# Optimization experiments

Hardware: AMD Instinct MI355X
Metric: run time of the kernel (lower is better)

## Reference

```python
import jax, jax.numpy as jnp
import numpy as np

D_PRIME = 512
D = 2048
CLASSES = 4


def setup_inputs() -> dict:
    key = jax.random.key(0)
    k1, k2, k3, k4 = jax.random.split(key, 4)
    N = 32768
    V_prime = jax.random.normal(k1, (N, D), dtype=jnp.float32)
    U_t = jax.random.normal(k2, (D_PRIME, D), dtype=jnp.float32)
    W_mta = jax.random.normal(k3, (1, D_PRIME), dtype=jnp.float32)
    W = jax.random.normal(k4, (CLASSES, D), dtype=jnp.float32)
    return {"V_prime": V_prime, "U_t": U_t, "W_mta": W_mta, "W": W}


def reference(V_prime, U_t, W_mta, W):
    # [D_prime, N] = tanh(U_t @ V'^T)
    tanh_scores = jnp.tanh(U_t @ V_prime.T)
    # attention over instances: [1, N]
    a = jax.nn.softmax(W_mta @ tanh_scores, axis=1)
    # weighted sum pooling: [D]
    t = jnp.sum(a.T * V_prime, axis=0)
    # final linear: [1, classes]
    l = (W @ t).reshape(1, CLASSES)
    return l
```

## Files before the change

kernel.cpp:

```cpp
#include <hip/hip_runtime.h>

#define N_INST 32768
#define DIM    2048
#define DP     512
#define NCLS   4

typedef _Float16 half8_t  __attribute__((ext_vector_type(8)));
typedef float    float4_t __attribute__((ext_vector_type(4)));

#define OFF_UHI   0ull
#define OFF_S     (OFF_UHI  + (size_t)DP*DIM*2)
#define OFF_STAT  (OFF_S    + (size_t)N_INST*4)

__device__ __forceinline__ float tanh_fast(float x) {
  float e = __expf(2.0f * x);
  return 1.0f - 2.0f / (e + 1.0f);
}

typedef const unsigned int __attribute__((address_space(1)))* gas_t;
typedef unsigned int       __attribute__((address_space(3)))* las_t;
__device__ __forceinline__ void gl16(const void* g, void* l) {
  __builtin_amdgcn_global_load_lds((gas_t)g, (las_t)l, 16, 0, 0);
}

__global__ __launch_bounds__(256) void k_cvt(const float4* __restrict__ in,
                                             half8_t* __restrict__ out,
                                             float4* __restrict__ s4z) {
  int i = blockIdx.x * 256 + threadIdx.x;
  float4 a = in[2 * i], b = in[2 * i + 1];
  half8_t h;
  h[0] = (_Float16)a.x; h[1] = (_Float16)a.y;
  h[2] = (_Float16)a.z; h[3] = (_Float16)a.w;
  h[4] = (_Float16)b.x; h[5] = (_Float16)b.y;
  h[6] = (_Float16)b.z; h[7] = (_Float16)b.w;
  out[i] = h;
  if (i < N_INST / 4) s4z[i] = make_float4(0.f, 0.f, 0.f, 0.f);
}

__global__ __launch_bounds__(512, 2) void k_score_gemm(
    const _Float16* __restrict__ Uhi, const float* __restrict__ V,
    const float* __restrict__ Wmta, float* __restrict__ s) {
  __shared__ _Float16 lA[2][256 * 64];
  __shared__ _Float16 lB[2][256 * 64];

  const int tid  = threadIdx.x;
  const int lane = tid & 63;
  const int wv   = tid >> 6;
  const int waveM = wv >> 2;
  const int waveN = wv & 3;
  const int quad = lane >> 4;
  const int col  = lane & 15;

  const int b   = blockIdx.x;
  const int grp = b >> 4;
  const int win = b & 15;
  const int mb  = win >> 3;
  const int nb  = grp * 8 + (win & 7);

  const int aRow0  = mb * 256;
  const int bRow0  = nb * 256;
  const int kStart = (nb & 31) << 6;

  const int rsub = lane >> 3;
  const int sswz = (lane & 7) ^ rsub;
  const _Float16* gA[4];
  int dA[4];
#pragma unroll
  for (int i2 = 0; i2 < 4; ++i2) {
    const int c = wv * 4 + i2;
    gA[i2] = Uhi + (size_t)(aRow0 + c * 8 + rsub) * DIM + sswz * 8;
    dA[i2] = c * 512;
  }

  const int rw = tid >> 1;
  const int hw = tid & 1;
  const float* gB = V + (size_t)(bRow0 + rw) * DIM + hw * 32;
  int wOffB[4];
#pragma unroll
  for (int p = 0; p < 4; ++p)
    wOffB[p] = rw * 128 + ((((hw << 2) | p) ^ (rw & 7)) << 4);

  const int fsw = (quad ^ (col & 7)) << 4;
  int offA[8], offB[4];
#pragma unroll
  for (int mi = 0; mi < 8; ++mi)
    offA[mi] = (waveM * 128 + mi * 16 + col) * 128 + fsw;
#pragma unroll
  for (int ni = 0; ni < 4; ++ni)
    offB[ni] = (waveN * 64 + ni * 16 + col) * 128 + fsw;

  float4_t acc[8][4];
  const float4_t z4 = {0.f, 0.f, 0.f, 0.f};
#pragma unroll
  for (int i = 0; i < 8; i++)
#pragma unroll
    for (int j = 0; j < 4; j++) acc[i][j] = z4;

  float4 rb[8];

#define KOF(t) ((kStart + (t) * 64) & (DIM - 1))

#define LOADB(kk) do {                                                     \
    const float4* p4 = (const float4*)(gB + (kk));                         \
    _Pragma("unroll")                                                      \
    for (int j = 0; j < 8; ++j) rb[j] = p4[j];                             \
  } while (0)

#define WRITEB(CUR) do {                                                   \
    char* base = (char*)&lB[CUR][0];                                       \
    _Pragma("unroll")                                                      \
    for (int p = 0; p < 4; ++p) {                                          \
      const auto c0 = __builtin_amdgcn_cvt_pkrtz(rb[2*p].x,   rb[2*p].y);  \
      const auto c1 = __builtin_amdgcn_cvt_pkrtz(rb[2*p].z,   rb[2*p].w);  \
      const auto c2 = __builtin_amdgcn_cvt_pkrtz(rb[2*p+1].x, rb[2*p+1].y);\
      const auto c3 = __builtin_amdgcn_cvt_pkrtz(rb[2*p+1].z, rb[2*p+1].w);\
      half8_t h;                                                           \
      h[0] = (_Float16)c0[0]; h[1] = (_Float16)c0[1];                      \
      h[2] = (_Float16)c1[0]; h[3] = (_Float16)c1[1];                      \
      h[4] = (_Float16)c2[0]; h[5] = (_Float16)c2[1];                      \
      h[6] = (_Float16)c3[0]; h[7] = (_Float16)c3[1];                      \
      *(half8_t*)(base + wOffB[p]) = h;                                    \
    }                                                                      \
  } while (0)

#define STAGEA(CUR, kk) do {                                               \
    gl16(gA[0] + (kk), &lA[CUR][dA[0]]);                                   \
    gl16(gA[1] + (kk), &lA[CUR][dA[1]]);                                   \
    gl16(gA[2] + (kk), &lA[CUR][dA[2]]);                                   \
    gl16(gA[3] + (kk), &lA[CUR][dA[3]]);                                   \
  } while (0)

#define COMPUTE(CUR) do {                                                  \
    const char* pA = (const char*)&lA[CUR][0];                             \
    const char* pB = (const char*)&lB[CUR][0];                             \
    _Pragma("unroll")                                                      \
    for (int kh = 0; kh < 2; ++kh) {                                       \
      half8_t af[8], bf[4];                                                \
      _Pragma("unroll")                                                    \
      for (int mi = 0; mi < 8; ++mi)                                       \
        af[mi] = *(const half8_t*)(pA + (offA[mi] ^ (kh << 6)));           \
      _Pragma("unroll")                                                    \
      for (int ni = 0; ni < 4; ++ni)                                       \
        bf[ni] = *(const half8_t*)(pB + (offB[ni] ^ (kh << 6)));           \
      _Pragma("unroll")                                                    \
      for (int mi = 0; mi < 8; ++mi)                                       \
        _Pragma("unroll")                                                  \
        for (int ni = 0; ni < 4; ++ni)                                     \
          acc[mi][ni] = __builtin_amdgcn_mfma_f32_16x16x32_f16(            \
              af[mi], bf[ni], acc[mi][ni], 0, 0, 0);                       \
    }                                                                      \
  } while (0)

  LOADB(KOF(0));
  STAGEA(0, KOF(0));
  WRITEB(0);
  LOADB(KOF(1));
  __syncthreads();

  for (int t = 0; t < 32; t += 2) {
    if (t < 31)  { STAGEA(1, KOF(t + 1)); WRITEB(1); }
    if (t < 30)  LOADB(KOF(t + 2));
    COMPUTE(0);
    __syncthreads();
    if (t + 1 < 31) { STAGEA(0, KOF(t + 2)); WRITEB(0); }
    if (t + 1 < 30) LOADB(KOF(t + 3));
    COMPUTE(1);
    __syncthreads();
  }
#undef KOF
#undef LOADB
#undef WRITEB
#undef STAGEA
#undef COMPUTE

#pragma unroll
  for (int ni = 0; ni < 4; ni++) {
    float v = 0.0f;
#pragma unroll
    for (int mi = 0; mi < 8; mi++) {
      const int jb = aRow0 + waveM * 128 + mi * 16 + quad * 4;
      union { float4_t v4; float f[4]; } u;
      u.v4 = acc[mi][ni];
#pragma unroll
      for (int r = 0; r < 4; r++)
        v += Wmta[jb + r] * tanh_fast(u.f[r]);
    }
    v += __shfl_xor(v, 16);
    v += __shfl_xor(v, 32);
    if (quad == 0) {
      const int n = bRow0 + waveN * 64 + ni * 16 + col;
      atomicAdd(&s[n], v);
    }
  }
}

__global__ __launch_bounds__(1024) void k_stats(const float* __restrict__ s,
                                                float* __restrict__ stats,
                                                float* __restrict__ out) {
  const int tid = threadIdx.x;
  const int lane = tid & 63;
  const int wvi = tid >> 6;
  __shared__ float smM[16], smP[16];
  const float4* s4 = (const float4*)s;

  if (tid < NCLS) out[tid] = 0.f;

  float m = -3.4e38f, p = 0.0f;
#pragma unroll
  for (int j = 0; j < 8; ++j) {
    float4 v = s4[tid * 8 + j];
    float lm = fmaxf(fmaxf(v.x, v.y), fmaxf(v.z, v.w));
    float lp = __expf(v.x - lm) + __expf(v.y - lm) +
               __expf(v.z - lm) + __expf(v.w - lm);
    float nm = fmaxf(m, lm);
    p = p * __expf(m - nm) + lp * __expf(lm - nm);
    m = nm;
  }
  for (int o = 32; o > 0; o >>= 1) {
    float om = __shfl_xor(m, o);
    float op = __shfl_xor(p, o);
    float nm = fmaxf(m, om);
    p = p * __expf(m - nm) + op * __expf(om - nm);
    m = nm;
  }
  if (lane == 0) { smM[wvi] = m; smP[wvi] = p; }
  __syncthreads();
  if (tid == 0) {
    float gm = smM[0];
    for (int w = 1; w < 16; w++) gm = fmaxf(gm, smM[w]);
    float sum = 0.f;
    for (int w = 0; w < 16; w++) sum += smP[w] * __expf(smM[w] - gm);
    stats[0] = gm;
    stats[1] = 1.0f / sum;
  }
}

__global__ __launch_bounds__(256) void k_pool(const float* __restrict__ V,
                                              const float* __restrict__ s,
                                              const float* __restrict__ stats,
                                              const float* __restrict__ W,
                                              float* __restrict__ out) {
  __shared__ float wsm[128];
  __shared__ int hot;
  __shared__ float sred[4][NCLS];
  const int tid = threadIdx.x;
  if (tid == 0) hot = 0;
  __syncthreads();
  const float mx = stats[0], inv = stats[1];
  const int n0 = blockIdx.x * 128;
  if (tid < 128) {
    const float w = __expf(s[n0 + tid] - mx) * inv;
    wsm[tid] = w;
    if (w > 1e-12f) atomicOr(&hot, 1);
  }
  __syncthreads();
  if (hot == 0) return;

  float acc[8] = {0.f, 0.f, 0.f, 0.f, 0.f, 0.f, 0.f, 0.f};
  for (int r = 0; r < 128; ++r) {
    const float w = wsm[r];
    if (w > 1e-12f) {
      const float4* vp = (const float4*)&V[(size_t)(n0 + r) * DIM + tid * 8];
      float4 va = vp[0], vb = vp[1];
      acc[0] += w * va.x; acc[1] += w * va.y; acc[2] += w * va.z; acc[3] += w * va.w;
      acc[4] += w * vb.x; acc[5] += w * vb.y; acc[6] += w * vb.z; acc[7] += w * vb.w;
    }
  }
  float pc[NCLS];
#pragma unroll
  for (int c = 0; c < NCLS; ++c) {
    const float4* w4 = (const float4*)&W[(size_t)c * DIM + tid * 8];
    const float4 wa = w4[0], wb = w4[1];
    pc[c] = wa.x * acc[0] + wa.y * acc[1] + wa.z * acc[2] + wa.w * acc[3] +
            wb.x * acc[4] + wb.y * acc[5] + wb.z * acc[6] + wb.w * acc[7];
  }
  const int lane = tid & 63, wvi = tid >> 6;
#pragma unroll
  for (int c = 0; c < NCLS; ++c)
    for (int o = 32; o > 0; o >>= 1) pc[c] += __shfl_xor(pc[c], o);
  if (lane == 0)
#pragma unroll
    for (int c = 0; c < NCLS; ++c) sred[wvi][c] = pc[c];
  __syncthreads();
  if (tid < NCLS)
    atomicAdd(&out[tid], sred[0][tid] + sred[1][tid] +
                         sred[2][tid] + sred[3][tid]);
}

extern "C" void kernel_launch(void* const* d_in, const int* in_sizes, int n_in,
                              void* d_out, int out_size, void* d_ws, size_t ws_size,
                              hipStream_t stream) {
  const float* Vp   = (const float*)d_in[0];
  const float* Ut   = (const float*)d_in[1];
  const float* Wmta = (const float*)d_in[2];
  const float* W    = (const float*)d_in[3];
  float* out = (float*)d_out;

  char* ws = (char*)d_ws;
  _Float16* Uhi  = (_Float16*)(ws + OFF_UHI);
  float*    sBuf = (float*)(ws + OFF_S);
  float*    stat = (float*)(ws + OFF_STAT);

  k_cvt<<<(DP * DIM / 8) / 256, 256, 0, stream>>>((const float4*)Ut,
                                                  (half8_t*)Uhi,
                                                  (float4*)sBuf);
  k_score_gemm<<<(DP / 256) * (N_INST / 256), 512, 0, stream>>>(Uhi, Vp, Wmta, sBuf);
  k_stats<<<1, 1024, 0, stream>>>(sBuf, stat, out);
  k_pool<<<N_INST / 128, 256, 0, stream>>>(Vp, sBuf, stat, W, out);
}
```

Before: 439.7 us.

## Shrink GEMM tiles to 128x128, drop score atomics, fuse stats into pool

```diff
diff --git a/kernel.cpp b/kernel.cpp
--- a/kernel.cpp
+++ b/kernel.cpp
@@ -9,8 +9,9 @@
 typedef float    float4_t __attribute__((ext_vector_type(4)));
 
 #define OFF_UHI   0ull
-#define OFF_S     (OFF_UHI  + (size_t)DP*DIM*2)
-#define OFF_STAT  (OFF_S    + (size_t)N_INST*4)
+#define OFF_SP    (OFF_UHI + (size_t)DP*DIM*2)
+#define OFF_PSTAT (OFF_SP  + (size_t)4*N_INST*4)
+#define OFF_CTL   (OFF_PSTAT + 4096ull)
 
 __device__ __forceinline__ float tanh_fast(float x) {
   float e = __expf(2.0f * x);
@@ -24,8 +25,9 @@
 }
 
 __global__ __launch_bounds__(256) void k_cvt(const float4* __restrict__ in,
-                                             half8_t* __restrict__ out,
-                                             float4* __restrict__ s4z) {
+                                             half8_t* __restrict__ outU,
+                                             int* __restrict__ ctl,
+                                             float* __restrict__ outv) {
   int i = blockIdx.x * 256 + threadIdx.x;
   float4 a = in[2 * i], b = in[2 * i + 1];
   half8_t h;
@@ -33,32 +35,35 @@
   h[2] = (_Float16)a.z; h[3] = (_Float16)a.w;
   h[4] = (_Float16)b.x; h[5] = (_Float16)b.y;
   h[6] = (_Float16)b.z; h[7] = (_Float16)b.w;
-  out[i] = h;
-  if (i < N_INST / 4) s4z[i] = make_float4(0.f, 0.f, 0.f, 0.f);
-}
-
-__global__ __launch_bounds__(512, 2) void k_score_gemm(
+  outU[i] = h;
+  if (i == 0) {
+    ctl[0] = 0; ctl[1] = 0;
+    outv[0] = 0.f; outv[1] = 0.f; outv[2] = 0.f; outv[3] = 0.f;
+  }
+}
+
+__global__ __launch_bounds__(256, 2) void k_score_gemm(
     const _Float16* __restrict__ Uhi, const float* __restrict__ V,
-    const float* __restrict__ Wmta, float* __restrict__ s) {
-  __shared__ _Float16 lA[2][256 * 64];
-  __shared__ _Float16 lB[2][256 * 64];
+    const float* __restrict__ Wmta, float* __restrict__ sP) {
+  __shared__ _Float16 lA[2][128 * 64];
+  __shared__ _Float16 lB[2][128 * 64];
 
   const int tid  = threadIdx.x;
   const int lane = tid & 63;
   const int wv   = tid >> 6;
-  const int waveM = wv >> 2;
-  const int waveN = wv & 3;
+  const int waveM = wv >> 1;
+  const int waveN = wv & 1;
   const int quad = lane >> 4;
   const int col  = lane & 15;
 
   const int b   = blockIdx.x;
-  const int grp = b >> 4;
-  const int win = b & 15;
+  const int grp = b >> 5;
+  const int win = b & 31;
   const int mb  = win >> 3;
   const int nb  = grp * 8 + (win & 7);
 
-  const int aRow0  = mb * 256;
-  const int bRow0  = nb * 256;
+  const int aRow0  = mb * 128;
+  const int bRow0  = nb * 128;
   const int kStart = (nb & 31) << 6;
 
   const int rsub = lane >> 3;
@@ -81,18 +86,18 @@
     wOffB[p] = rw * 128 + ((((hw << 2) | p) ^ (rw & 7)) << 4);
 
   const int fsw = (quad ^ (col & 7)) << 4;
-  int offA[8], offB[4];
-#pragma unroll
-  for (int mi = 0; mi < 8; ++mi)
-    offA[mi] = (waveM * 128 + mi * 16 + col) * 128 + fsw;
+  int offA[4], offB[4];
+#pragma unroll
+  for (int mi = 0; mi < 4; ++mi)
+    offA[mi] = (waveM * 64 + mi * 16 + col) * 128 + fsw;
 #pragma unroll
   for (int ni = 0; ni < 4; ++ni)
     offB[ni] = (waveN * 64 + ni * 16 + col) * 128 + fsw;
 
-  float4_t acc[8][4];
+  float4_t acc[4][4];
   const float4_t z4 = {0.f, 0.f, 0.f, 0.f};
 #pragma unroll
-  for (int i = 0; i < 8; i++)
+  for (int i = 0; i < 4; i++)
 #pragma unroll
     for (int j = 0; j < 4; j++) acc[i][j] = z4;
 
@@ -135,15 +140,15 @@
     const char* pB = (const char*)&lB[CUR][0];                             \
     _Pragma("unroll")                                                      \
     for (int kh = 0; kh < 2; ++kh) {                                       \
-      half8_t af[8], bf[4];                                                \
+      half8_t af[4], bf[4];                                                \
       _Pragma("unroll")                                                    \
-      for (int mi = 0; mi < 8; ++mi)                                       \
+      for (int mi = 0; mi < 4; ++mi)                                       \
         af[mi] = *(const half8_t*)(pA + (offA[mi] ^ (kh << 6)));           \
       _Pragma("unroll")                                                    \
       for (int ni = 0; ni < 4; ++ni)                                       \
         bf[ni] = *(const half8_t*)(pB + (offB[ni] ^ (kh << 6)));           \
       _Pragma("unroll")                                                    \
-      for (int mi = 0; mi < 8; ++mi)                                       \
+      for (int mi = 0; mi < 4; ++mi)                                       \
         _Pragma("unroll")                                                  \
         for (int ni = 0; ni < 4; ++ni)                                     \
           acc[mi][ni] = __builtin_amdgcn_mfma_f32_16x16x32_f16(            \
@@ -173,12 +178,13 @@
 #undef STAGEA
 #undef COMPUTE
 
+  float vout[4];
 #pragma unroll
   for (int ni = 0; ni < 4; ni++) {
     float v = 0.0f;
 #pragma unroll
-    for (int mi = 0; mi < 8; mi++) {
-      const int jb = aRow0 + waveM * 128 + mi * 16 + quad * 4;
+    for (int mi = 0; mi < 4; mi++) {
+      const int jb = aRow0 + waveM * 64 + mi * 16 + quad * 4;
       union { float4_t v4; float f[4]; } u;
       u.v4 = acc[mi][ni];
 #pragma unroll
@@ -187,38 +193,49 @@
     }
     v += __shfl_xor(v, 16);
     v += __shfl_xor(v, 32);
-    if (quad == 0) {
+    vout[ni] = v;
+  }
+  float* sred = (float*)&lA[0][0];
+  if (waveM == 0 && quad == 0) {
+#pragma unroll
+    for (int ni = 0; ni < 4; ni++)
+      sred[waveN * 64 + ni * 16 + col] = vout[ni];
+  }
+  __syncthreads();
+  if (waveM == 1 && quad == 0) {
+#pragma unroll
+    for (int ni = 0; ni < 4; ni++) {
       const int n = bRow0 + waveN * 64 + ni * 16 + col;
-      atomicAdd(&s[n], v);
-    }
-  }
-}
-
-__global__ __launch_bounds__(1024) void k_stats(const float* __restrict__ s,
-                                                float* __restrict__ stats,
-                                                float* __restrict__ out) {
-  const int tid = threadIdx.x;
-  const int lane = tid & 63;
-  const int wvi = tid >> 6;
-  __shared__ float smM[16], smP[16];
-  const float4* s4 = (const float4*)s;
-
-  if (tid < NCLS) out[tid] = 0.f;
+      sP[(size_t)mb * N_INST + n] = vout[ni] + sred[waveN * 64 + ni * 16 + col];
+    }
+  }
+}
+
+__global__ __launch_bounds__(256) void k_tail(const float* __restrict__ sP,
+                                              const float* __restrict__ V,
+                                              const float* __restrict__ W,
+                                              float* __restrict__ pstat,
+                                              int* __restrict__ ctl,
+                                              float* __restrict__ out) {
+  __shared__ float wsm[128];
+  __shared__ float smM[4], smP[4];
+  __shared__ float gstat[2];
+  __shared__ float sredc[4][NCLS];
+  __shared__ int isLast, hot;
+  const int tid = threadIdx.x, lane = tid & 63, wvi = tid >> 6;
+  const int n0 = blockIdx.x * 128;
+
+  if (tid == 0) { isLast = 0; hot = 0; }
 
   float m = -3.4e38f, p = 0.0f;
-#pragma unroll
-  for (int j = 0; j < 8; ++j) {
-    float4 v = s4[tid * 8 + j];
-    float lm = fmaxf(fmaxf(v.x, v.y), fmaxf(v.z, v.w));
-    float lp = __expf(v.x - lm) + __expf(v.y - lm) +
-               __expf(v.z - lm) + __expf(v.w - lm);
-    float nm = fmaxf(m, lm);
-    p = p * __expf(m - nm) + lp * __expf(lm - nm);
-    m = nm;
+  if (tid < 128) {
+    float sv = sP[n0 + tid] + sP[N_INST + n0 + tid] +
+               sP[2 * N_INST + n0 + tid] + sP[3 * N_INST + n0 + tid];
+    wsm[tid] = sv;
+    m = sv; p = 1.0f;
   }
   for (int o = 32; o > 0; o >>= 1) {
-    float om = __shfl_xor(m, o);
-    float op = __shfl_xor(p, o);
+    float om = __shfl_xor(m, o), op = __shfl_xor(p, o);
     float nm = fmaxf(m, om);
     p = p * __expf(m - nm) + op * __expf(om - nm);
     m = nm;
@@ -226,30 +243,53 @@
   if (lane == 0) { smM[wvi] = m; smP[wvi] = p; }
   __syncthreads();
   if (tid == 0) {
-    float gm = smM[0];
-    for (int w = 1; w < 16; w++) gm = fmaxf(gm, smM[w]);
-    float sum = 0.f;
-    for (int w = 0; w < 16; w++) sum += smP[w] * __expf(smM[w] - gm);
-    stats[0] = gm;
-    stats[1] = 1.0f / sum;
-  }
-}
-
-__global__ __launch_bounds__(256) void k_pool(const float* __restrict__ V,
-                                              const float* __restrict__ s,
-                                              const float* __restrict__ stats,
-                                              const float* __restrict__ W,
-                                              float* __restrict__ out) {
-  __shared__ float wsm[128];
-  __shared__ int hot;
-  __shared__ float sred[4][NCLS];
-  const int tid = threadIdx.x;
-  if (tid == 0) hot = 0;
-  __syncthreads();
-  const float mx = stats[0], inv = stats[1];
-  const int n0 = blockIdx.x * 128;
+    float bm = smM[0], bp = smP[0];
+    for (int w2 = 1; w2 < 4; ++w2) {
+      float nm = fmaxf(bm, smM[w2]);
+      bp = bp * __expf(bm - nm) + smP[w2] * __expf(smM[w2] - nm);
+      bm = nm;
+    }
+    pstat[blockIdx.x * 2]     = bm;
+    pstat[blockIdx.x * 2 + 1] = bp;
+    __threadfence();
+    if (atomicAdd(&ctl[0], 1) == 255) isLast = 1;
+  }
+  __syncthreads();
+
+  if (isLast) {
+    __threadfence();
+    float m2 = pstat[2 * tid], p2 = pstat[2 * tid + 1];
+    for (int o = 32; o > 0; o >>= 1) {
+      float om = __shfl_xor(m2, o), op = __shfl_xor(p2, o);
+      float nm = fmaxf(m2, om);
+      p2 = p2 * __expf(m2 - nm) + op * __expf(om - nm);
+      m2 = nm;
+    }
+    if (lane == 0) { smM[wvi] = m2; smP[wvi] = p2; }
+    __syncthreads();
+    if (tid == 0) {
+      float gm = smM[0], gp = smP[0];
+      for (int w2 = 1; w2 < 4; ++w2) {
+        float nm = fmaxf(gm, smM[w2]);
+        gp = gp * __expf(gm - nm) + smP[w2] * __expf(smM[w2] - nm);
+        gm = nm;
+      }
+      pstat[512] = gm;
+      pstat[513] = 1.0f / gp;
+      __threadfence();
+      atomicExch(&ctl[1], 1);
+    }
+  }
+
+  if (tid == 0) {
+    while (atomicAdd(&ctl[1], 0) == 0) __builtin_amdgcn_s_sleep(8);
+    __threadfence();
+    gstat[0] = pstat[512]; gstat[1] = pstat[513];
+  }
+  __syncthreads();
+  const float mx = gstat[0], inv = gstat[1];
   if (tid < 128) {
-    const float w = __expf(s[n0 + tid] - mx) * inv;
+    const float w = __expf(wsm[tid] - mx) * inv;
     wsm[tid] = w;
     if (w > 1e-12f) atomicOr(&hot, 1);
   }
@@ -274,17 +314,16 @@
     pc[c] = wa.x * acc[0] + wa.y * acc[1] + wa.z * acc[2] + wa.w * acc[3] +
             wb.x * acc[4] + wb.y * acc[5] + wb.z * acc[6] + wb.w * acc[7];
   }
-  const int lane = tid & 63, wvi = tid >> 6;
 #pragma unroll
   for (int c = 0; c < NCLS; ++c)
     for (int o = 32; o > 0; o >>= 1) pc[c] += __shfl_xor(pc[c], o);
   if (lane == 0)
 #pragma unroll
-    for (int c = 0; c < NCLS; ++c) sred[wvi][c] = pc[c];
+    for (int c = 0; c < NCLS; ++c) sredc[wvi][c] = pc[c];
   __syncthreads();
   if (tid < NCLS)
-    atomicAdd(&out[tid], sred[0][tid] + sred[1][tid] +
-                         sred[2][tid] + sred[3][tid]);
+    atomicAdd(&out[tid], sredc[0][tid] + sredc[1][tid] +
+                         sredc[2][tid] + sredc[3][tid]);
 }
 
 extern "C" void kernel_launch(void* const* d_in, const int* in_sizes, int n_in,
@@ -298,13 +337,12 @@
 
   char* ws = (char*)d_ws;
   _Float16* Uhi  = (_Float16*)(ws + OFF_UHI);
-  float*    sBuf = (float*)(ws + OFF_S);
-  float*    stat = (float*)(ws + OFF_STAT);
+  float*    sP   = (float*)(ws + OFF_SP);
+  float*    pstat= (float*)(ws + OFF_PSTAT);
+  int*      ctl  = (int*)(ws + OFF_CTL);
 
   k_cvt<<<(DP * DIM / 8) / 256, 256, 0, stream>>>((const float4*)Ut,
-                                                  (half8_t*)Uhi,
-                                                  (float4*)sBuf);
-  k_score_gemm<<<(DP / 256) * (N_INST / 256), 512, 0, stream>>>(Uhi, Vp, Wmta, sBuf);
-  k_stats<<<1, 1024, 0, stream>>>(sBuf, stat, out);
-  k_pool<<<N_INST / 128, 256, 0, stream>>>(Vp, sBuf, stat, W, out);
-}
+                                                  (half8_t*)Uhi, ctl, out);
+  k_score_gemm<<<(DP / 128) * (N_INST / 128), 256, 0, stream>>>(Uhi, Vp, Wmta, sP);
+  k_tail<<<N_INST / 128, 256, 0, stream>>>(sP, Vp, W, pstat, ctl, out);
+}
```

Result: slower. 507.9 us (+15.5%).
